# Optimization experiments

Hardware: AMD Instinct MI355X
Metric: run time of the kernel (lower is better)

## Reference

```python
import jax, jax.numpy as jnp
import numpy as np

DEPTH, DIM, M_DIM, K = 3, 16, 16, 8  # depth, emb_dim, EGNN m_dim default, num_nearest_neighbors
LN_EPS = 1e-5


def _gather(x, idx):
    # x: [B,L,...], idx: [B,L,K] -> [B,L,K,...] (per-batch neighbor gather)
    return jax.vmap(lambda xb, ib: xb[ib])(x, idx)


def _lin(k, fi, fo):
    k1, k2 = jax.random.split(k)
    lim = 1.0 / np.sqrt(fi)
    w = jax.random.uniform(k1, (fi, fo), minval=-lim, maxval=lim, dtype=jnp.float32)
    b = jax.random.uniform(k2, (fo,), minval=-lim, maxval=lim, dtype=jnp.float32)
    return w, b


def _stacked(k, fi, fo):
    ws, bs = zip(*[_lin(kk, fi, fo) for kk in jax.random.split(k, DEPTH)])
    return jnp.stack(ws), jnp.stack(bs)


def setup_inputs() -> dict:
    key = jax.random.key(0)
    ks = jax.random.split(key, 16)
    B, L, num_tokens = 16, 1024, 2
    edge_in = 2 * DIM + 1  # feats_i, feats_j, rel_dist
    inp = {}
    inp['coords'] = jax.random.normal(ks[0], (B, L, 3), dtype=jnp.float32) * 3.0
    inp['residues'] = jax.random.randint(ks[1], (B, L), 0, num_tokens)
    inp['lengths'] = jax.random.randint(ks[2], (B,), L // 2, L + 1)
    inp['token_emb'] = jax.random.normal(ks[3], (num_tokens, DIM), dtype=jnp.float32)
    inp['pos_emb'] = jax.random.normal(ks[4], (L, DIM), dtype=jnp.float32)
    inp['edge_w1'], inp['edge_b1'] = _stacked(ks[5], edge_in, edge_in * 2)
    inp['edge_w2'], inp['edge_b2'] = _stacked(ks[6], edge_in * 2, M_DIM)
    inp['coors_w1'], inp['coors_b1'] = _stacked(ks[7], M_DIM, M_DIM * 4)
    inp['coors_w2'], inp['coors_b2'] = _stacked(ks[8], M_DIM * 4, 1)
    inp['ln_g'] = jnp.ones((DEPTH, DIM), jnp.float32)
    inp['ln_b'] = jnp.zeros((DEPTH, DIM), jnp.float32)
    inp['node_w1'], inp['node_b1'] = _stacked(ks[9], DIM + M_DIM, DIM * 2)
    inp['node_w2'], inp['node_b2'] = _stacked(ks[10], DIM * 2, DIM)
    inp['final_w'], inp['final_b'] = _lin(ks[11], DIM, 3)
    return inp


def reference(coords, residues, lengths, token_emb, pos_emb,
              edge_w1, edge_b1, edge_w2, edge_b2,
              coors_w1, coors_b1, coors_w2, coors_b2,
              ln_g, ln_b, node_w1, node_b1, node_w2, node_b2,
              final_w, final_b):
    B, L, _ = coords.shape
    silu = jax.nn.silu
    mask = jnp.arange(L)[None, :] < lengths[:, None]                 # [B,L]
    pair_mask = mask[:, :, None] & mask[:, None, :]                  # [B,L,L]
    eye = jnp.eye(L, dtype=bool)
    # chain adjacency: i <-> i+1 where both endpoints are within length
    r = jnp.arange(L - 1)
    chain = jnp.zeros((L, L), bool).at[r, r + 1].set(True)
    chain = chain | chain.T
    adj = (chain[None] & pair_mask) & ~eye                           # [B,L,L]

    feats = token_emb[residues] + pos_emb[None, :L]                  # [B,L,D]
    coors = coords
    for d in range(DEPTH):
        # pairwise squared distances for kNN ranking (memory-bound)
        rel_dist_full = jnp.sum((coors[:, :, None] - coors[:, None, :]) ** 2, -1)  # [B,L,L]
        ranking = jnp.where(pair_mask, rel_dist_full, 1e5)
        ranking = jnp.where(eye, -1.0, ranking)   # self always selected first
        ranking = jnp.where(adj, 0.0, ranking)    # adjacency edges forced in
        _, idx = jax.lax.top_k(-ranking, K)                           # [B,L,K] smallest
        mask_j = _gather(mask, idx)
        emask = mask[:, :, None] & mask_j                             # [B,L,K] (valid_radius=inf)
        coors_j = _gather(coors, idx)                                 # [B,L,K,3]
        rel_coors = coors[:, :, None] - coors_j                       # [B,L,K,3]
        rel_dist = jnp.sum(rel_coors ** 2, -1, keepdims=True)         # [B,L,K,1]
        feats_j = _gather(feats, idx)                                 # [B,L,K,D]
        feats_i = jnp.broadcast_to(feats[:, :, None], feats_j.shape)
        edge_in = jnp.concatenate([feats_i, feats_j, rel_dist], -1)   # [B,L,K,2D+1]
        h = silu(edge_in @ edge_w1[d] + edge_b1[d])
        m_ij = silu(h @ edge_w2[d] + edge_b2[d])                      # [B,L,K,M]
        # equivariant coordinate update
        w = silu(m_ij @ coors_w1[d] + coors_b1[d]) @ coors_w2[d] + coors_b2[d]
        w = jnp.where(emask[..., None], w, 0.0)[..., 0]               # [B,L,K]
        coors = coors + jnp.einsum('blk,blkc->blc', w, rel_coors)
        # node update (norm_feats=True in EGNN_Network -> LayerNorm)
        m_i = jnp.sum(jnp.where(emask[..., None], m_ij, 0.0), 2)      # [B,L,M]
        mu = feats.mean(-1, keepdims=True)
        var = jnp.mean((feats - mu) ** 2, -1, keepdims=True)
        normed = (feats - mu) / jnp.sqrt(var + LN_EPS) * ln_g[d] + ln_b[d]
        nin = jnp.concatenate([normed, m_i], -1)                      # [B,L,D+M]
        feats = feats + (silu(nin @ node_w1[d] + node_b1[d]) @ node_w2[d] + node_b2[d])
    delta = feats @ final_w + final_b                                 # [B,L,3]
    return delta
```

## Files before the change

kernel.cpp:

```cpp
#include <hip/hip_runtime.h>
#include <math.h>

typedef unsigned long long u64;
typedef unsigned int u32;

#define NB 16
#define SL 1024
#define DIM 16
#define MDIM 16
#define KNN 8
#define EH 66
#define CH 64
#define NHID 32
#define LN_EPS 1e-5f
#define W1T_STRIDE 36
#define ABSTRIDE 72

__device__ __forceinline__ float silu_f(float x) {
    return x / (1.0f + __expf(-x));
}

__global__ __launch_bounds__(256) void init_kernel(
    const float* __restrict__ coords, const int* __restrict__ residues,
    const float* __restrict__ token_emb, const float* __restrict__ pos_emb,
    float* __restrict__ coordsA, float* __restrict__ featsA)
{
    const int nid = blockIdx.x * 256 + threadIdx.x;
    if (nid >= NB * SL) return;
    const int l = nid & (SL - 1);
    const int r = residues[nid];
#pragma unroll
    for (int c = 0; c < DIM; ++c)
        featsA[nid * DIM + c] = token_emb[r * DIM + c] + pos_emb[l * DIM + c];
#pragma unroll
    for (int c = 0; c < 3; ++c)
        coordsA[nid * 3 + c] = coords[nid * 3 + c];
}

__global__ __launch_bounds__(256) void pack_kernel(
    const float* __restrict__ ew1, const float* __restrict__ cw1,
    const float* __restrict__ nw1, const float* __restrict__ nw2,
    float* __restrict__ w1t, float* __restrict__ cw1t,
    float* __restrict__ nw1t, float* __restrict__ nw2t)
{
    const int stride = gridDim.x * 256;
    const int t0 = blockIdx.x * 256 + threadIdx.x;
    for (int idx = t0; idx < 3 * EH * 33; idx += stride) {
        int d = idx / (EH * 33); int r = idx - d * EH * 33; int u = r / 33; int c = r - u * 33;
        w1t[(d * EH + u) * W1T_STRIDE + c] = ew1[(d * 33 + c) * EH + u];
    }
    for (int idx = t0; idx < 3 * CH * 16; idx += stride) {
        int d = idx / (CH * 16); int r = idx - d * CH * 16; int t = r >> 4; int v = r & 15;
        cw1t[(d * CH + t) * 16 + v] = cw1[(d * 16 + v) * CH + t];
    }
    for (int idx = t0; idx < 3 * NHID * 32; idx += stride) {
        int d = idx / (NHID * 32); int r = idx - d * NHID * 32; int u = r >> 5; int c = r & 31;
        nw1t[(d * NHID + u) * 32 + c] = nw1[(d * 32 + c) * NHID + u];
    }
    for (int idx = t0; idx < 3 * 16 * 32; idx += stride) {
        int d = idx / (16 * 32); int r = idx - d * 16 * 32; int c = r >> 5; int u = r & 31;
        nw2t[(d * 16 + c) * 32 + u] = nw2[(d * 32 + u) * 16 + c];
    }
}

__global__ __launch_bounds__(256) void nodepre_kernel(
    const int d, const float* __restrict__ featsIn,
    const float* __restrict__ w1t, const float* __restrict__ g_eb1,
    float* __restrict__ Atab, float* __restrict__ Btab)
{
    __shared__ float s_w1[EH * W1T_STRIDE];
    __shared__ float s_eb1[EH];
    const int tid = threadIdx.x;
    for (int t = tid; t < EH * W1T_STRIDE; t += 256) s_w1[t] = w1t[d * EH * W1T_STRIDE + t];
    if (tid < EH) s_eb1[tid] = g_eb1[d * EH + tid];
    __syncthreads();

    const int t0 = blockIdx.x * 256 + tid;
    const int n = t0 >> 1;
    const int h = t0 & 1;
    float f[16];
    {
        const float4* pp = (const float4*)(featsIn + (size_t)n * DIM);
        float4 a = pp[0], c2 = pp[1], c3 = pp[2], c4 = pp[3];
        f[0]=a.x; f[1]=a.y; f[2]=a.z; f[3]=a.w;
        f[4]=c2.x; f[5]=c2.y; f[6]=c2.z; f[7]=c2.w;
        f[8]=c3.x; f[9]=c3.y; f[10]=c3.z; f[11]=c3.w;
        f[12]=c4.x; f[13]=c4.y; f[14]=c4.z; f[15]=c4.w;
    }
    const int ub = h * 33;
    float* Ao = Atab + (size_t)n * ABSTRIDE + 36 * h;
    float* Bo = Btab + (size_t)n * ABSTRIDE + 36 * h;
#pragma unroll 3
    for (int t = 0; t < 33; ++t) {
        const float* wr = &s_w1[(ub + t) * W1T_STRIDE];
        float a0 = s_eb1[ub + t], a1 = 0.f, b0 = 0.f, b1 = 0.f;
#pragma unroll
        for (int c = 0; c < 16; c += 2) {
            a0 = fmaf(f[c],     wr[c],          a0);
            a1 = fmaf(f[c + 1], wr[c + 1],      a1);
            b0 = fmaf(f[c],     wr[16 + c],     b0);
            b1 = fmaf(f[c + 1], wr[16 + c + 1], b1);
        }
        Ao[t] = a0 + a1;
        Bo[t] = b0 + b1;
    }
}

#define CSU(x, y) { u32 mn = min(lst[x], lst[y]); u32 mx = max(lst[x], lst[y]); lst[x] = mn; lst[y] = mx; }

__global__ __launch_bounds__(1024) void knn_kernel(
    const float* __restrict__ coords, const int* __restrict__ lengths,
    int* __restrict__ idxbuf)
{
    __shared__ float4 s_cand4[SL];
    const int tid = threadIdx.x;
    const int b = blockIdx.x >> 6;
    const int i0 = (blockIdx.x & 63) << 4;
    const int len = lengths[b];
    const float* cb = coords + (size_t)b * SL * 3;
    {
        const int idx = tid;
        s_cand4[idx] = make_float4(cb[idx * 3 + 0], cb[idx * 3 + 1], cb[idx * 3 + 2], 0.0f);
    }
    __syncthreads();

    const int wv = tid >> 6;
    const int lane = tid & 63;
    const int i = i0 + wv;
    const float4 ciq = s_cand4[i];
    const float xi = ciq.x, yi = ciq.y, zi = ciq.z;

    u32 lst[8];
#pragma unroll
    for (int t = 0; t < 8; ++t) lst[t] = 0xFFFFFFFFu;

#pragma unroll 4
    for (int t = 0; t < 16; ++t) {
        const int j = t * 64 + lane;
        const float4 cj = s_cand4[j];
        const float dx = xi - cj.x, dy = yi - cj.y, dz = zi - cj.z;
        const float dist = dx * dx + dy * dy + dz * dz;
        const bool valid = j < len;
        const u32 kd = (__float_as_uint(dist) | 0x80000000u) & 0xFFFFFC00u;
        u32 key = valid ? kd : 0xC7C35000u;
        if (valid && (j == i + 1 || j + 1 == i)) key = 0x80000000u;
        if (j == i) key = 0x407FFC00u;
        key |= (u32)j;
#pragma unroll
        for (int p = 7; p >= 1; --p)
            lst[p] = (key < lst[p]) ? ((key < lst[p - 1]) ? lst[p - 1] : key) : lst[p];
        lst[0] = min(key, lst[0]);
    }

#pragma unroll
    for (int m = 1; m < 64; m <<= 1) {
        u32 o[8];
#pragma unroll
        for (int t = 0; t < 8; ++t) o[t] = (u32)__shfl_xor((int)lst[7 - t], m, 64);
#pragma unroll
        for (int t = 0; t < 8; ++t) lst[t] = min(lst[t], o[t]);
        CSU(0, 4) CSU(1, 5) CSU(2, 6) CSU(3, 7)
        CSU(0, 2) CSU(1, 3) CSU(4, 6) CSU(5, 7)
        CSU(0, 1) CSU(2, 3) CSU(4, 5) CSU(6, 7)
    }

    if (lane == 0) {
        const size_t node = (size_t)b * SL + i;
        int4 r0 = make_int4((int)(lst[0] & 1023u), (int)(lst[1] & 1023u), (int)(lst[2] & 1023u), (int)(lst[3] & 1023u));
        int4 r1 = make_int4((int)(lst[4] & 1023u), (int)(lst[5] & 1023u), (int)(lst[6] & 1023u), (int)(lst[7] & 1023u));
        ((int4*)idxbuf)[node * 2 + 0] = r0;
        ((int4*)idxbuf)[node * 2 + 1] = r1;
    }
}

__global__ __launch_bounds__(256, 5) void layer_kernel(
    const int d,
    const float* __restrict__ coordsIn, float* __restrict__ coordsOut,
    const float* __restrict__ featsIn, float* __restrict__ featsOut,
    const int* __restrict__ idxbuf, const int* __restrict__ lengths,
    const float* __restrict__ Atab, const float* __restrict__ Btab,
    const float* __restrict__ w1t,
    const float* __restrict__ g_ew2, const float* __restrict__ g_eb2,
    const float* __restrict__ cw1t, const float* __restrict__ g_cb1,
    const float* __restrict__ g_cw2, const float* __restrict__ g_cb2,
    const float* __restrict__ g_lng, const float* __restrict__ g_lnb,
    const float* __restrict__ nw1t, const float* __restrict__ g_nb1,
    const float* __restrict__ nw2t, const float* __restrict__ g_nb2)
{
    __shared__ float s_w2e[EH * 16];
    __shared__ float s_w1c[EH];
    __shared__ float s_cw1[CH * 16];
    __shared__ float s_cw2v[CH];
    __shared__ float s_cb1[CH];
    __shared__ float s_nw1[NHID * 36];
    __shared__ float s_nw2[16 * 36];
    __shared__ float s_eb2[16];
    __shared__ float s_lng[16], s_lnb[16], s_nb1[32], s_nb2[16];
    __shared__ float s_cb2v;
    __shared__ float s_buf[2][16][66];
    __shared__ float s_wx[2][2][64];

    const int tid = threadIdx.x;
    for (int t = tid; t < EH * 16; t += 256) s_w2e[t] = g_ew2[d * EH * 16 + t];
    for (int t = tid; t < CH * 16; t += 256) s_cw1[t] = cw1t[d * CH * 16 + t];
    for (int t = tid; t < NHID * 32; t += 256) s_nw1[(t >> 5) * 36 + (t & 31)] = nw1t[d * NHID * 32 + t];
    for (int t = tid; t < 16 * 32; t += 256) s_nw2[(t >> 5) * 36 + (t & 31)] = nw2t[d * 16 * 32 + t];
    if (tid < CH) { s_cw2v[tid] = g_cw2[d * CH + tid]; s_cb1[tid] = g_cb1[d * CH + tid]; }
    if (tid < EH) s_w1c[tid] = w1t[d * EH * W1T_STRIDE + tid * W1T_STRIDE + 32];
    if (tid >= 128 && tid < 144) {
        const int c = tid - 128;
        s_eb2[c] = g_eb2[d * 16 + c];
        s_lng[c] = g_lng[d * 16 + c];
        s_lnb[c] = g_lnb[d * 16 + c];
        s_nb2[c] = g_nb2[d * 16 + c];
    }
    if (tid >= 160 && tid < 192) s_nb1[tid - 160] = g_nb1[d * 32 + (tid - 160)];
    if (tid == 200) s_cb2v = g_cb2[d];

    const int wv = tid >> 6;
    const int g = wv >> 1;
    const int h = wv & 1;
    const int lane = tid & 63;
    const int e = blockIdx.x * 128 + g * 64 + lane;
    const int n = e >> 3;
    const int b = n >> 10;
    const int i = n & (SL - 1);
    const int k = lane & 7;
    const int len = lengths[b];
    const int j = idxbuf[e];
    const bool em = (i < len) && (j < len);

    float ci[3], rel[3];
    {
        const float* cp = coordsIn + (size_t)n * 3;
        const float* cq = coordsIn + ((size_t)b * SL + j) * 3;
        ci[0] = cp[0]; ci[1] = cp[1]; ci[2] = cp[2];
        rel[0] = ci[0] - cq[0]; rel[1] = ci[1] - cq[1]; rel[2] = ci[2] - cq[2];
    }
    const float rd = fmaf(rel[0], rel[0], fmaf(rel[1], rel[1], rel[2] * rel[2]));

    float fi[16];
    if (h) {
        const float4* pp = (const float4*)(featsIn + (size_t)n * DIM);
        float4 a = pp[0], c2 = pp[1], c3 = pp[2], c4 = pp[3];
        fi[0]=a.x; fi[1]=a.y; fi[2]=a.z; fi[3]=a.w;
        fi[4]=c2.x; fi[5]=c2.y; fi[6]=c2.z; fi[7]=c2.w;
        fi[8]=c3.x; fi[9]=c3.y; fi[10]=c3.z; fi[11]=c3.w;
        fi[12]=c4.x; fi[13]=c4.y; fi[14]=c4.z; fi[15]=c4.w;
    }

    const float4* Aq = (const float4*)(Atab + (size_t)n * ABSTRIDE + 36 * h);
    const float4* Bq = (const float4*)(Btab + ((size_t)b * SL + j) * ABSTRIDE + 36 * h);

    __syncthreads();

    const int ub = h * 33;
    float macc[16];
#pragma unroll
    for (int v = 0; v < 16; ++v) macc[v] = h ? 0.0f : s_eb2[v];
#pragma unroll
    for (int c = 0; c < 9; ++c) {
        const float4 a4 = Aq[c];
        const float4 b4 = Bq[c];
        const float av[4] = {a4.x, a4.y, a4.z, a4.w};
        const float bv[4] = {b4.x, b4.y, b4.z, b4.w};
#pragma unroll
        for (int q = 0; q < 4; ++q) {
            const int t = 4 * c + q;
            if (t < 33) {
                const float hin = fmaf(rd, s_w1c[ub + t], av[q] + bv[q]);
                const float hh = silu_f(hin);
                const float* w2r = &s_w2e[(ub + t) * 16];
#pragma unroll
                for (int v = 0; v < 16; ++v) macc[v] = fmaf(hh, w2r[v], macc[v]);
            }
        }
    }

    if (h) {
#pragma unroll
        for (int v = 0; v < 16; ++v) s_buf[g][v][lane] = macc[v];
    }
    __syncthreads();
    float mm[16];
    if (!h) {
#pragma unroll
        for (int v = 0; v < 16; ++v) { macc[v] += s_buf[g][v][lane]; mm[v] = silu_f(macc[v]); s_buf[g][v][lane] = mm[v]; }
    }
    __syncthreads();
    if (h) {
#pragma unroll
        for (int v = 0; v < 16; ++v) mm[v] = s_buf[g][v][lane];
    }

    {
        const int tb = h * 32;
        float wa = 0.f;
#pragma unroll 4
        for (int tt = 0; tt < 32; ++tt) {
            const float* cr = &s_cw1[(tb + tt) * 16];
            float a0 = s_cb1[tb + tt], a1 = 0.f;
#pragma unroll
            for (int v = 0; v < 16; v += 2) {
                a0 = fmaf(mm[v], cr[v], a0);
                a1 = fmaf(mm[v + 1], cr[v + 1], a1);
            }
            wa = fmaf(silu_f(a0 + a1), s_cw2v[tb + tt], wa);
        }
        s_wx[g][h][lane] = wa;
    }
    __syncthreads();

    if (!h) {
        const float we = em ? (s_wx[g][0][lane] + s_wx[g][1][lane] + s_cb2v) : 0.f;
        float wr0 = we * rel[0], wr1 = we * rel[1], wr2 = we * rel[2];
#pragma unroll
        for (int s = 1; s < 8; s <<= 1) {
            wr0 += __shfl_xor(wr0, s, 64);
            wr1 += __shfl_xor(wr1, s, 64);
            wr2 += __shfl_xor(wr2, s, 64);
        }
        if (k == 0) {
            coordsOut[(size_t)n * 3 + 0] = ci[0] + wr0;
            coordsOut[(size_t)n * 3 + 1] = ci[1] + wr1;
            coordsOut[(size_t)n * 3 + 2] = ci[2] + wr2;
        }
    } else {
        float mi_[16];
#pragma unroll
        for (int v = 0; v < 16; ++v) mi_[v] = em ? mm[v] : 0.f;
#pragma unroll
        for (int s = 1; s < 8; s <<= 1) {
#pragma unroll
            for (int v = 0; v < 16; ++v) mi_[v] += __shfl_xor(mi_[v], s, 64);
        }
        float mu = 0.f;
#pragma unroll
        for (int c = 0; c < 16; ++c) mu += fi[c];
        mu *= 0.0625f;
        float var = 0.f;
#pragma unroll
        for (int c = 0; c < 16; ++c) { const float dd = fi[c] - mu; var = fmaf(dd, dd, var); }
        var *= 0.0625f;
        const float rs = rsqrtf(var + LN_EPS);
        float nn[16];
#pragma unroll
        for (int c = 0; c < 16; ++c) nn[c] = fmaf((fi[c] - mu) * rs, s_lng[c], s_lnb[c]);

        float nh[4];
#pragma unroll
        for (int qq = 0; qq < 4; ++qq) {
            const int u = k * 4 + qq;
            const float* nr = &s_nw1[u * 36];
            float a0 = s_nb1[u], a1 = 0.f;
#pragma unroll
            for (int c = 0; c < 16; c += 2) {
                a0 = fmaf(nn[c], nr[c], a0);
                a1 = fmaf(nn[c + 1], nr[c + 1], a1);
            }
#pragma unroll
            for (int v = 0; v < 16; v += 2) {
                a0 = fmaf(mi_[v], nr[16 + v], a0);
                a1 = fmaf(mi_[v + 1], nr[16 + v + 1], a1);
            }
            nh[qq] = silu_f(a0 + a1);
        }
        const int c0 = 2 * k, c1 = 2 * k + 1;
        const float* w2a = &s_nw2[c0 * 36];
        const float* w2b = &s_nw2[c1 * 36];
        float o0 = s_nb2[c0], o1 = s_nb2[c1];
        const int lbase = lane & ~7;
#pragma unroll
        for (int u = 0; u < 32; ++u) {
            const float v = __shfl(nh[u & 3], lbase + (u >> 2), 64);
            o0 = fmaf(v, w2a[u], o0);
            o1 = fmaf(v, w2b[u], o1);
        }
        ((float2*)featsOut)[(size_t)n * 8 + k] = make_float2(fi[c0] + o0, fi[c1] + o1);
    }
}

__global__ __launch_bounds__(256) void final_kernel(
    const float* __restrict__ feats, const float* __restrict__ fw,
    const float* __restrict__ fb, float* __restrict__ out)
{
    const int nid = blockIdx.x * 256 + threadIdx.x;
    if (nid >= NB * SL) return;
    float f[DIM];
#pragma unroll
    for (int c = 0; c < DIM; ++c) f[c] = feats[nid * DIM + c];
#pragma unroll
    for (int o = 0; o < 3; ++o) {
        float acc = fb[o];
#pragma unroll
        for (int c = 0; c < DIM; ++c) acc = fmaf(f[c], fw[c * 3 + o], acc);
        out[nid * 3 + o] = acc;
    }
}

extern "C" void kernel_launch(void* const* d_in, const int* in_sizes, int n_in,
                              void* d_out, int out_size, void* d_ws, size_t ws_size,
                              hipStream_t stream) {
    const float* coords    = (const float*)d_in[0];
    const int*   residues  = (const int*)d_in[1];
    const int*   lengths   = (const int*)d_in[2];
    const float* token_emb = (const float*)d_in[3];
    const float* pos_emb   = (const float*)d_in[4];
    const float* ew1 = (const float*)d_in[5];
    const float* eb1 = (const float*)d_in[6];
    const float* ew2 = (const float*)d_in[7];
    const float* eb2 = (const float*)d_in[8];
    const float* cw1 = (const float*)d_in[9];
    const float* cb1 = (const float*)d_in[10];
    const float* cw2 = (const float*)d_in[11];
    const float* cb2 = (const float*)d_in[12];
    const float* lng = (const float*)d_in[13];
    const float* lnb = (const float*)d_in[14];
    const float* nw1 = (const float*)d_in[15];
    const float* nb1 = (const float*)d_in[16];
    const float* nw2 = (const float*)d_in[17];
    const float* nb2 = (const float*)d_in[18];
    const float* fw  = (const float*)d_in[19];
    const float* fb  = (const float*)d_in[20];

    float* ws = (float*)d_ws;
    float* coordsA = ws;
    float* coordsB = coordsA + NB * SL * 3;
    float* featsA  = coordsB + NB * SL * 3;
    float* featsB  = featsA + NB * SL * DIM;
    int*   idxbuf  = (int*)(featsB + NB * SL * DIM);
    float* w1t  = (float*)(idxbuf + NB * SL * KNN);
    float* cw1t = w1t + 3 * EH * W1T_STRIDE;
    float* nw1t = cw1t + 3 * CH * 16;
    float* nw2t = nw1t + 3 * NHID * 32;
    float* Atab = nw2t + 3 * 16 * 32;
    float* Btab = Atab + (size_t)NB * SL * ABSTRIDE;

    pack_kernel<<<32, 256, 0, stream>>>(ew1, cw1, nw1, nw2, w1t, cw1t, nw1t, nw2t);
    init_kernel<<<NB * SL / 256, 256, 0, stream>>>(coords, residues, token_emb, pos_emb, coordsA, featsA);

    float* cIn = coordsA; float* cOut = coordsB;
    float* fIn = featsA;  float* fOut = featsB;
    for (int d = 0; d < 3; ++d) {
        knn_kernel<<<NB * 64, 1024, 0, stream>>>(cIn, lengths, idxbuf);
        nodepre_kernel<<<NB * SL * 2 / 256, 256, 0, stream>>>(d, fIn, w1t, eb1, Atab, Btab);
        layer_kernel<<<NB * SL * KNN / 128, 256, 0, stream>>>(d, cIn, cOut, fIn, fOut, idxbuf, lengths,
            Atab, Btab, w1t, ew2, eb2, cw1t, cb1, cw2, cb2, lng, lnb, nw1t, nb1, nw2t, nb2);
        float* t;
        t = cIn; cIn = cOut; cOut = t;
        t = fIn; fIn = fOut; fOut = t;
    }

    final_kernel<<<NB * SL / 256, 256, 0, stream>>>(fIn, fw, fb, (float*)d_out);
}
```

Measured before the change: 307.6 us.

## Fuse next-layer node precompute and final projection into layer kernel; batch KNN queries

The per-layer nodepre launch is removed for layers 1 and 2: the end of layer_kernel now computes the next layer's A/B edge tables from the freshly updated features. It writes them into a second, double-buffered pair of tables. The final linear projection is folded into the last layer using a shuffle reduction, and the separate final kernel is gone. knn_kernel now handles two query points per wavefront, halving the block count. Most small weight arrays are read straight from global memory instead of being staged in LDS, and one barrier is dropped. The cost is extra register and LDS pressure in layer_kernel, plus a larger workspace for the second pair of A/B tables.

```diff
diff --git a/kernel.cpp b/kernel.cpp
--- a/kernel.cpp
+++ b/kernel.cpp
@@ -69,10 +69,8 @@
     float* __restrict__ Atab, float* __restrict__ Btab)
 {
     __shared__ float s_w1[EH * W1T_STRIDE];
-    __shared__ float s_eb1[EH];
     const int tid = threadIdx.x;
     for (int t = tid; t < EH * W1T_STRIDE; t += 256) s_w1[t] = w1t[d * EH * W1T_STRIDE + t];
-    if (tid < EH) s_eb1[tid] = g_eb1[d * EH + tid];
     __syncthreads();
 
     const int t0 = blockIdx.x * 256 + tid;
@@ -93,7 +91,7 @@
 #pragma unroll 3
     for (int t = 0; t < 33; ++t) {
         const float* wr = &s_w1[(ub + t) * W1T_STRIDE];
-        float a0 = s_eb1[ub + t], a1 = 0.f, b0 = 0.f, b1 = 0.f;
+        float a0 = g_eb1[d * EH + ub + t], a1 = 0.f, b0 = 0.f, b1 = 0.f;
 #pragma unroll
         for (int c = 0; c < 16; c += 2) {
             a0 = fmaf(f[c],     wr[c],          a0);
@@ -108,66 +106,80 @@
 
 #define CSU(x, y) { u32 mn = min(lst[x], lst[y]); u32 mx = max(lst[x], lst[y]); lst[x] = mn; lst[y] = mx; }
 
-__global__ __launch_bounds__(1024) void knn_kernel(
+__device__ __forceinline__ void butterfly8(u32* lst) {
+#pragma unroll
+    for (int m = 1; m < 64; m <<= 1) {
+        u32 o[8];
+#pragma unroll
+        for (int t = 0; t < 8; ++t) o[t] = (u32)__shfl_xor((int)lst[7 - t], m, 64);
+#pragma unroll
+        for (int t = 0; t < 8; ++t) lst[t] = min(lst[t], o[t]);
+        CSU(0, 4) CSU(1, 5) CSU(2, 6) CSU(3, 7)
+        CSU(0, 2) CSU(1, 3) CSU(4, 6) CSU(5, 7)
+        CSU(0, 1) CSU(2, 3) CSU(4, 5) CSU(6, 7)
+    }
+}
+
+__device__ __forceinline__ void ins8(u32* lst, u32 key) {
+#pragma unroll
+    for (int p = 7; p >= 1; --p)
+        lst[p] = (key < lst[p]) ? ((key < lst[p - 1]) ? lst[p - 1] : key) : lst[p];
+    lst[0] = min(key, lst[0]);
+}
+
+__device__ __forceinline__ u32 mk_key(int j, int i, int len, float dist) {
+    const bool valid = j < len;
+    const u32 kd = (__float_as_uint(dist) | 0x80000000u) & 0xFFFFFC00u;
+    u32 key = valid ? kd : 0xC7C35000u;
+    if (valid && (j == i + 1 || j + 1 == i)) key = 0x80000000u;
+    if (j == i) key = 0x407FFC00u;
+    return key | (u32)j;
+}
+
+__global__ __launch_bounds__(1024, 8) void knn_kernel(
     const float* __restrict__ coords, const int* __restrict__ lengths,
     int* __restrict__ idxbuf)
 {
     __shared__ float4 s_cand4[SL];
     const int tid = threadIdx.x;
-    const int b = blockIdx.x >> 6;
-    const int i0 = (blockIdx.x & 63) << 4;
+    const int b = blockIdx.x >> 5;
+    const int i0 = (blockIdx.x & 31) << 5;
     const int len = lengths[b];
     const float* cb = coords + (size_t)b * SL * 3;
-    {
-        const int idx = tid;
-        s_cand4[idx] = make_float4(cb[idx * 3 + 0], cb[idx * 3 + 1], cb[idx * 3 + 2], 0.0f);
-    }
+    s_cand4[tid] = make_float4(cb[tid * 3 + 0], cb[tid * 3 + 1], cb[tid * 3 + 2], 0.0f);
     __syncthreads();
 
     const int wv = tid >> 6;
     const int lane = tid & 63;
-    const int i = i0 + wv;
-    const float4 ciq = s_cand4[i];
-    const float xi = ciq.x, yi = ciq.y, zi = ciq.z;
-
-    u32 lst[8];
-#pragma unroll
-    for (int t = 0; t < 8; ++t) lst[t] = 0xFFFFFFFFu;
+    const int iA = i0 + 2 * wv;
+    const int iB = iA + 1;
+    const float4 cA = s_cand4[iA];
+    const float4 cB = s_cand4[iB];
+
+    u32 lstA[8], lstB[8];
+#pragma unroll
+    for (int t = 0; t < 8; ++t) { lstA[t] = 0xFFFFFFFFu; lstB[t] = 0xFFFFFFFFu; }
 
 #pragma unroll 4
     for (int t = 0; t < 16; ++t) {
         const int j = t * 64 + lane;
         const float4 cj = s_cand4[j];
-        const float dx = xi - cj.x, dy = yi - cj.y, dz = zi - cj.z;
-        const float dist = dx * dx + dy * dy + dz * dz;
-        const bool valid = j < len;
-        const u32 kd = (__float_as_uint(dist) | 0x80000000u) & 0xFFFFFC00u;
-        u32 key = valid ? kd : 0xC7C35000u;
-        if (valid && (j == i + 1 || j + 1 == i)) key = 0x80000000u;
-        if (j == i) key = 0x407FFC00u;
-        key |= (u32)j;
-#pragma unroll
-        for (int p = 7; p >= 1; --p)
-            lst[p] = (key < lst[p]) ? ((key < lst[p - 1]) ? lst[p - 1] : key) : lst[p];
-        lst[0] = min(key, lst[0]);
-    }
-
-#pragma unroll
-    for (int m = 1; m < 64; m <<= 1) {
-        u32 o[8];
-#pragma unroll
-        for (int t = 0; t < 8; ++t) o[t] = (u32)__shfl_xor((int)lst[7 - t], m, 64);
-#pragma unroll
-        for (int t = 0; t < 8; ++t) lst[t] = min(lst[t], o[t]);
-        CSU(0, 4) CSU(1, 5) CSU(2, 6) CSU(3, 7)
-        CSU(0, 2) CSU(1, 3) CSU(4, 6) CSU(5, 7)
-        CSU(0, 1) CSU(2, 3) CSU(4, 5) CSU(6, 7)
-    }
-
-    if (lane == 0) {
-        const size_t node = (size_t)b * SL + i;
-        int4 r0 = make_int4((int)(lst[0] & 1023u), (int)(lst[1] & 1023u), (int)(lst[2] & 1023u), (int)(lst[3] & 1023u));
-        int4 r1 = make_int4((int)(lst[4] & 1023u), (int)(lst[5] & 1023u), (int)(lst[6] & 1023u), (int)(lst[7] & 1023u));
+        const float dxA = cA.x - cj.x, dyA = cA.y - cj.y, dzA = cA.z - cj.z;
+        const float dxB = cB.x - cj.x, dyB = cB.y - cj.y, dzB = cB.z - cj.z;
+        const float dA = dxA * dxA + dyA * dyA + dzA * dzA;
+        const float dB = dxB * dxB + dyB * dyB + dzB * dzB;
+        ins8(lstA, mk_key(j, iA, len, dA));
+        ins8(lstB, mk_key(j, iB, len, dB));
+    }
+
+    butterfly8(lstA);
+    butterfly8(lstB);
+
+    if (lane < 2) {
+        const u32* l = lane ? lstB : lstA;
+        const size_t node = (size_t)b * SL + (lane ? iB : iA);
+        int4 r0 = make_int4((int)(l[0] & 1023u), (int)(l[1] & 1023u), (int)(l[2] & 1023u), (int)(l[3] & 1023u));
+        int4 r1 = make_int4((int)(l[4] & 1023u), (int)(l[5] & 1023u), (int)(l[6] & 1023u), (int)(l[7] & 1023u));
         ((int4*)idxbuf)[node * 2 + 0] = r0;
         ((int4*)idxbuf)[node * 2 + 1] = r1;
     }
@@ -178,44 +190,30 @@
     const float* __restrict__ coordsIn, float* __restrict__ coordsOut,
     const float* __restrict__ featsIn, float* __restrict__ featsOut,
     const int* __restrict__ idxbuf, const int* __restrict__ lengths,
-    const float* __restrict__ Atab, const float* __restrict__ Btab,
-    const float* __restrict__ w1t,
+    const float* __restrict__ Ain, const float* __restrict__ Bin,
+    float* __restrict__ Aout, float* __restrict__ Bout,
+    const float* __restrict__ w1t, const float* __restrict__ g_eb1,
     const float* __restrict__ g_ew2, const float* __restrict__ g_eb2,
     const float* __restrict__ cw1t, const float* __restrict__ g_cb1,
     const float* __restrict__ g_cw2, const float* __restrict__ g_cb2,
     const float* __restrict__ g_lng, const float* __restrict__ g_lnb,
     const float* __restrict__ nw1t, const float* __restrict__ g_nb1,
-    const float* __restrict__ nw2t, const float* __restrict__ g_nb2)
+    const float* __restrict__ nw2t, const float* __restrict__ g_nb2,
+    const float* __restrict__ fw, const float* __restrict__ fb,
+    float* __restrict__ out)
 {
-    __shared__ float s_w2e[EH * 16];
-    __shared__ float s_w1c[EH];
-    __shared__ float s_cw1[CH * 16];
-    __shared__ float s_cw2v[CH];
-    __shared__ float s_cb1[CH];
+    __shared__ float s_buf[2][16][66];
+    __shared__ float s_wx[2][2][64];
     __shared__ float s_nw1[NHID * 36];
     __shared__ float s_nw2[16 * 36];
-    __shared__ float s_eb2[16];
-    __shared__ float s_lng[16], s_lnb[16], s_nb1[32], s_nb2[16];
-    __shared__ float s_cb2v;
-    __shared__ float s_buf[2][16][66];
-    __shared__ float s_wx[2][2][64];
+    __shared__ float s_w1n[EH * 36];
 
     const int tid = threadIdx.x;
-    for (int t = tid; t < EH * 16; t += 256) s_w2e[t] = g_ew2[d * EH * 16 + t];
-    for (int t = tid; t < CH * 16; t += 256) s_cw1[t] = cw1t[d * CH * 16 + t];
     for (int t = tid; t < NHID * 32; t += 256) s_nw1[(t >> 5) * 36 + (t & 31)] = nw1t[d * NHID * 32 + t];
     for (int t = tid; t < 16 * 32; t += 256) s_nw2[(t >> 5) * 36 + (t & 31)] = nw2t[d * 16 * 32 + t];
-    if (tid < CH) { s_cw2v[tid] = g_cw2[d * CH + tid]; s_cb1[tid] = g_cb1[d * CH + tid]; }
-    if (tid < EH) s_w1c[tid] = w1t[d * EH * W1T_STRIDE + tid * W1T_STRIDE + 32];
-    if (tid >= 128 && tid < 144) {
-        const int c = tid - 128;
-        s_eb2[c] = g_eb2[d * 16 + c];
-        s_lng[c] = g_lng[d * 16 + c];
-        s_lnb[c] = g_lnb[d * 16 + c];
-        s_nb2[c] = g_nb2[d * 16 + c];
-    }
-    if (tid >= 160 && tid < 192) s_nb1[tid - 160] = g_nb1[d * 32 + (tid - 160)];
-    if (tid == 200) s_cb2v = g_cb2[d];
+    if (d < 2) {
+        for (int t = tid; t < EH * 36; t += 256) s_w1n[t] = w1t[(d + 1) * EH * 36 + t];
+    }
 
     const int wv = tid >> 6;
     const int g = wv >> 1;
@@ -249,15 +247,16 @@
         fi[12]=c4.x; fi[13]=c4.y; fi[14]=c4.z; fi[15]=c4.w;
     }
 
-    const float4* Aq = (const float4*)(Atab + (size_t)n * ABSTRIDE + 36 * h);
-    const float4* Bq = (const float4*)(Btab + ((size_t)b * SL + j) * ABSTRIDE + 36 * h);
-
-    __syncthreads();
+    const float4* Aq = (const float4*)(Ain + (size_t)n * ABSTRIDE + 36 * h);
+    const float4* Bq = (const float4*)(Bin + ((size_t)b * SL + j) * ABSTRIDE + 36 * h);
 
     const int ub = h * 33;
+    const float* w1base = w1t + ((size_t)d * EH + ub) * W1T_STRIDE;
+    const float* w2base = g_ew2 + ((size_t)d * EH + ub) * 16;
+    const float* eb2r = g_eb2 + d * 16;
     float macc[16];
 #pragma unroll
-    for (int v = 0; v < 16; ++v) macc[v] = h ? 0.0f : s_eb2[v];
+    for (int v = 0; v < 16; ++v) macc[v] = h ? 0.0f : eb2r[v];
 #pragma unroll
     for (int c = 0; c < 9; ++c) {
         const float4 a4 = Aq[c];
@@ -268,9 +267,9 @@
         for (int q = 0; q < 4; ++q) {
             const int t = 4 * c + q;
             if (t < 33) {
-                const float hin = fmaf(rd, s_w1c[ub + t], av[q] + bv[q]);
+                const float hin = fmaf(rd, w1base[t * W1T_STRIDE + 32], av[q] + bv[q]);
                 const float hh = silu_f(hin);
-                const float* w2r = &s_w2e[(ub + t) * 16];
+                const float* w2r = w2base + t * 16;
 #pragma unroll
                 for (int v = 0; v < 16; ++v) macc[v] = fmaf(hh, w2r[v], macc[v]);
             }
@@ -295,24 +294,27 @@
 
     {
         const int tb = h * 32;
+        const float* c1base = cw1t + ((size_t)d * CH + tb) * 16;
+        const float* cb1r = g_cb1 + d * CH + tb;
+        const float* cw2r = g_cw2 + d * CH + tb;
         float wa = 0.f;
 #pragma unroll 4
         for (int tt = 0; tt < 32; ++tt) {
-            const float* cr = &s_cw1[(tb + tt) * 16];
-            float a0 = s_cb1[tb + tt], a1 = 0.f;
+            const float* cr = c1base + tt * 16;
+            float a0 = cb1r[tt], a1 = 0.f;
 #pragma unroll
             for (int v = 0; v < 16; v += 2) {
                 a0 = fmaf(mm[v], cr[v], a0);
                 a1 = fmaf(mm[v + 1], cr[v + 1], a1);
             }
-            wa = fmaf(silu_f(a0 + a1), s_cw2v[tb + tt], wa);
+            wa = fmaf(silu_f(a0 + a1), cw2r[tt], wa);
         }
         s_wx[g][h][lane] = wa;
     }
     __syncthreads();
 
     if (!h) {
-        const float we = em ? (s_wx[g][0][lane] + s_wx[g][1][lane] + s_cb2v) : 0.f;
+        const float we = em ? (s_wx[g][0][lane] + s_wx[g][1][lane] + g_cb2[d]) : 0.f;
         float wr0 = we * rel[0], wr1 = we * rel[1], wr2 = we * rel[2];
 #pragma unroll
         for (int s = 1; s < 8; s <<= 1) {
@@ -345,14 +347,14 @@
         const float rs = rsqrtf(var + LN_EPS);
         float nn[16];
 #pragma unroll
-        for (int c = 0; c < 16; ++c) nn[c] = fmaf((fi[c] - mu) * rs, s_lng[c], s_lnb[c]);
+        for (int c = 0; c < 16; ++c) nn[c] = fmaf((fi[c] - mu) * rs, g_lng[d * 16 + c], g_lnb[d * 16 + c]);
 
         float nh[4];
 #pragma unroll
         for (int qq = 0; qq < 4; ++qq) {
             const int u = k * 4 + qq;
             const float* nr = &s_nw1[u * 36];
-            float a0 = s_nb1[u], a1 = 0.f;
+            float a0 = g_nb1[d * 32 + u], a1 = 0.f;
 #pragma unroll
             for (int c = 0; c < 16; c += 2) {
                 a0 = fmaf(nn[c], nr[c], a0);
@@ -368,7 +370,7 @@
         const int c0 = 2 * k, c1 = 2 * k + 1;
         const float* w2a = &s_nw2[c0 * 36];
         const float* w2b = &s_nw2[c1 * 36];
-        float o0 = s_nb2[c0], o1 = s_nb2[c1];
+        float o0 = g_nb2[d * 16 + c0], o1 = g_nb2[d * 16 + c1];
         const int lbase = lane & ~7;
 #pragma unroll
         for (int u = 0; u < 32; ++u) {
@@ -376,25 +378,52 @@
             o0 = fmaf(v, w2a[u], o0);
             o1 = fmaf(v, w2b[u], o1);
         }
-        ((float2*)featsOut)[(size_t)n * 8 + k] = make_float2(fi[c0] + o0, fi[c1] + o1);
-    }
-}
-
-__global__ __launch_bounds__(256) void final_kernel(
-    const float* __restrict__ feats, const float* __restrict__ fw,
-    const float* __restrict__ fb, float* __restrict__ out)
-{
-    const int nid = blockIdx.x * 256 + threadIdx.x;
-    if (nid >= NB * SL) return;
-    float f[DIM];
-#pragma unroll
-    for (int c = 0; c < DIM; ++c) f[c] = feats[nid * DIM + c];
-#pragma unroll
-    for (int o = 0; o < 3; ++o) {
-        float acc = fb[o];
-#pragma unroll
-        for (int c = 0; c < DIM; ++c) acc = fmaf(f[c], fw[c * 3 + o], acc);
-        out[nid * 3 + o] = acc;
+        const float nf0 = fi[c0] + o0;
+        const float nf1 = fi[c1] + o1;
+
+        if (d == 2) {
+            float p0 = nf0 * fw[c0 * 3 + 0] + nf1 * fw[c1 * 3 + 0];
+            float p1 = nf0 * fw[c0 * 3 + 1] + nf1 * fw[c1 * 3 + 1];
+            float p2 = nf0 * fw[c0 * 3 + 2] + nf1 * fw[c1 * 3 + 2];
+#pragma unroll
+            for (int s = 1; s < 8; s <<= 1) {
+                p0 += __shfl_xor(p0, s, 64);
+                p1 += __shfl_xor(p1, s, 64);
+                p2 += __shfl_xor(p2, s, 64);
+            }
+            if (k == 0) {
+                out[(size_t)n * 3 + 0] = p0 + fb[0];
+                out[(size_t)n * 3 + 1] = p1 + fb[1];
+                out[(size_t)n * 3 + 2] = p2 + fb[2];
+            }
+        } else {
+            ((float2*)featsOut)[(size_t)n * 8 + k] = make_float2(nf0, nf1);
+            float f[16];
+#pragma unroll
+            for (int m = 0; m < 8; ++m) {
+                f[2 * m]     = __shfl(nf0, lbase + m, 64);
+                f[2 * m + 1] = __shfl(nf1, lbase + m, 64);
+            }
+#pragma unroll
+            for (int m = 0; m < 9; ++m) {
+                const int u = k + 8 * m;
+                if (u < EH) {
+                    const float* row = &s_w1n[u * 36];
+                    float a0 = g_eb1[(d + 1) * EH + u], a1 = 0.f, b0 = 0.f, b1 = 0.f;
+#pragma unroll
+                    for (int c = 0; c < 16; c += 2) {
+                        a0 = fmaf(f[c],     row[c],          a0);
+                        a1 = fmaf(f[c + 1], row[c + 1],      a1);
+                        b0 = fmaf(f[c],     row[16 + c],     b0);
+                        b1 = fmaf(f[c + 1], row[16 + c + 1], b1);
+                    }
+                    const int half = (u >= 33) ? 1 : 0;
+                    const size_t off = (size_t)n * ABSTRIDE + 36 * half + (u - 33 * half);
+                    Aout[off] = a0 + a1;
+                    Bout[off] = b0 + b1;
+                }
+            }
+        }
     }
 }
 
@@ -433,23 +462,28 @@
     float* cw1t = w1t + 3 * EH * W1T_STRIDE;
     float* nw1t = cw1t + 3 * CH * 16;
     float* nw2t = nw1t + 3 * NHID * 32;
-    float* Atab = nw2t + 3 * 16 * 32;
-    float* Btab = Atab + (size_t)NB * SL * ABSTRIDE;
+    float* Atab0 = nw2t + 3 * 16 * 32;
+    float* Btab0 = Atab0 + (size_t)NB * SL * ABSTRIDE;
+    float* Atab1 = Btab0 + (size_t)NB * SL * ABSTRIDE;
+    float* Btab1 = Atab1 + (size_t)NB * SL * ABSTRIDE;
 
     pack_kernel<<<32, 256, 0, stream>>>(ew1, cw1, nw1, nw2, w1t, cw1t, nw1t, nw2t);
     init_kernel<<<NB * SL / 256, 256, 0, stream>>>(coords, residues, token_emb, pos_emb, coordsA, featsA);
+    nodepre_kernel<<<NB * SL * 2 / 256, 256, 0, stream>>>(0, featsA, w1t, eb1, Atab0, Btab0);
 
     float* cIn = coordsA; float* cOut = coordsB;
     float* fIn = featsA;  float* fOut = featsB;
+    float* Ain = Atab0; float* Bin = Btab0;
+    float* Aout = Atab1; float* Bout = Btab1;
     for (int d = 0; d < 3; ++d) {
-        knn_kernel<<<NB * 64, 1024, 0, stream>>>(cIn, lengths, idxbuf);
-        nodepre_kernel<<<NB * SL * 2 / 256, 256, 0, stream>>>(d, fIn, w1t, eb1, Atab, Btab);
+        knn_kernel<<<NB * 32, 1024, 0, stream>>>(cIn, lengths, idxbuf);
         layer_kernel<<<NB * SL * KNN / 128, 256, 0, stream>>>(d, cIn, cOut, fIn, fOut, idxbuf, lengths,
-            Atab, Btab, w1t, ew2, eb2, cw1t, cb1, cw2, cb2, lng, lnb, nw1t, nb1, nw2t, nb2);
+            Ain, Bin, Aout, Bout, w1t, eb1, ew2, eb2, cw1t, cb1, cw2, cb2,
+            lng, lnb, nw1t, nb1, nw2t, nb2, fw, fb, (float*)d_out);
         float* t;
         t = cIn; cIn = cOut; cOut = t;
         t = fIn; fIn = fOut; fOut = t;
-    }
-
-    final_kernel<<<NB * SL / 256, 256, 0, stream>>>(fIn, fw, fb, (float*)d_out);
-}
+        t = Ain; Ain = Aout; Aout = t;
+        t = Bin; Bin = Bout; Bout = t;
+    }
+}
```

Result: slower. 351.8 us (+14.4%).
